# Kernel optimization log

Measured on AMD Instinct MI355X. Metric: run time of the kernel, lower is better.

Reference implementation:

```python
import jax, jax.numpy as jnp
import numpy as np

N, E, D, H = 50000, 800000, 64, 4  # nodes, edges, dim_embedding (=per-head channels), heads
NEG_SLOPE = 0.2
EPS = 1e-16


def _gat(x, src, dst, W, att_src, att_dst, bias, n):
    # x: [N, Din], W: [Din, H*D] -> per-head features [N, H, D]
    xw = (x @ W).reshape(n, H, D)
    a_src = jnp.einsum('nhc,hc->nh', xw, att_src)  # [N, H]
    a_dst = jnp.einsum('nhc,hc->nh', xw, att_dst)
    logits = jax.nn.leaky_relu(a_src[src] + a_dst[dst], NEG_SLOPE)  # [E, H]
    # segment softmax over incoming edges of each destination node
    m = jax.ops.segment_max(logits, dst, num_segments=n)  # [N, H]
    ex = jnp.exp(logits - m[dst])
    s = jax.ops.segment_sum(ex, dst, num_segments=n)
    alpha = ex / (s[dst] + EPS)  # [E, H]
    msg = xw[src] * alpha[..., None]  # [E, H, D]
    out = jax.ops.segment_sum(msg, dst, num_segments=n)  # [N, H, D]
    return out.mean(axis=1) + bias  # concat=False head-mean, [N, D]


def setup_inputs() -> dict:
    key = jax.random.key(0)
    ks = jax.random.split(key, 16)
    sc = 1.0 / np.sqrt(D)
    inp = {
        'x': jax.random.normal(ks[0], (N, D), jnp.float32),
        'edge_index': jax.random.randint(ks[1], (2, E), 0, N, jnp.int64),
    }
    for i, tag in ((2, '1'), (9, '2')):
        inp['W' + tag] = jax.random.normal(ks[i], (D, H * D), jnp.float32) * sc
        inp['att_src' + tag] = jax.random.normal(ks[i + 1], (H, D), jnp.float32) * sc
        inp['att_dst' + tag] = jax.random.normal(ks[i + 2], (H, D), jnp.float32) * sc
        inp['b' + tag] = jnp.zeros((D,), jnp.float32)
        inp['lW' + tag] = jax.random.normal(ks[i + 3], (D, D), jnp.float32) * sc
        inp['lb' + tag] = jnp.zeros((D,), jnp.float32)
    return inp


def reference(x, edge_index, W1, att_src1, att_dst1, b1, lW1, lb1,
              W2, att_src2, att_dst2, b2, lW2, lb2):
    src, dst = edge_index[0], edge_index[1]
    n = x.shape[0]
    h = _gat(x, src, dst, W1, att_src1, att_dst1, b1, n) + (x @ lW1 + lb1)
    h = jax.nn.relu(h)
    out = _gat(h, src, dst, W2, att_src2, att_dst2, b2, n) + (h @ lW2 + lb2)
    return out
```

## Files before the change

kernel.cpp:

```cpp
#include <hip/hip_runtime.h>
#include <math.h>

typedef __attribute__((ext_vector_type(8))) short short8;
typedef __attribute__((ext_vector_type(4))) float f32x4;

#define NBSH 9
#define MAXBIN 128

__device__ inline unsigned fenc(float f){
  unsigned u = __float_as_uint(f);
  return u ^ ((u >> 31) ? 0xFFFFFFFFu : 0x80000000u);
}
__device__ inline float fdec(unsigned k){
  unsigned u = (k & 0x80000000u) ? (k ^ 0x80000000u) : ~k;
  return __uint_as_float(u);
}
__device__ inline unsigned short bf16rne(float f){
  unsigned u = __float_as_uint(f);
  return (unsigned short)((u + 0x7FFFu + ((u >> 16) & 1u)) >> 16);
}

__global__ __launch_bounds__(256) void k_hist(const int* __restrict__ dst, int* __restrict__ deg, int E){
  int e = blockIdx.x*256 + threadIdx.x;
  if (e < E) atomicAdd(&deg[dst[e]], 1);
}

__global__ __launch_bounds__(256) void k_scan(const int* __restrict__ deg, int* __restrict__ offs,
    int* __restrict__ partials, int* __restrict__ flags, int* __restrict__ bincur,
    int nelem, int ndeg){
  __shared__ int sh[256];
  __shared__ int sh2[256];
  int t = threadIdx.x, b = blockIdx.x;
  int i = b*256 + t;
  int v = (i < ndeg) ? deg[i] : 0;
  sh[t] = v; __syncthreads();
  for (int d = 1; d < 256; d <<= 1){
    int add = (t >= d) ? sh[t-d] : 0; __syncthreads();
    sh[t] += add; __syncthreads();
  }
  if (t == 255){
    partials[b] = sh[255];
    __threadfence();
    atomicExch(&flags[b], 1);
  }
  int myp = 0;
  if (t < b){
    while (atomicAdd(&flags[t], 0) == 0){}
    myp = atomicAdd(&partials[t], 0);
  }
  __syncthreads();
  sh2[t] = myp; __syncthreads();
  #pragma unroll
  for (int d = 128; d >= 1; d >>= 1){
    if (t < d) sh2[t] += sh2[t + d];
    __syncthreads();
  }
  int off = sh2[0];
  if (i < nelem){
    int val = off + sh[t] - v;
    offs[i] = val;
    if (i < ndeg && (i & ((1<<NBSH)-1)) == 0) bincur[i >> NBSH] = val;
  }
}

__global__ __launch_bounds__(512) void k_prep(
    const float* __restrict__ W1, const float* __restrict__ as1, const float* __restrict__ ad1,
    const float* __restrict__ b1, const float* __restrict__ lb1, const float* __restrict__ lW1,
    const float* __restrict__ W2, const float* __restrict__ as2, const float* __restrict__ ad2,
    const float* __restrict__ b2, const float* __restrict__ lb2, const float* __restrict__ lW2,
    short* __restrict__ wbigT, short* __restrict__ wattBsw, float* __restrict__ bcomb,
    unsigned* __restrict__ gmax, int4* __restrict__ rec2, int* __restrict__ deg,
    int* __restrict__ flags, int E, int n){
  int L = blockIdx.x;
  const float* W   = L ? W2  : W1;
  const float* asv = L ? as2 : as1;
  const float* adv = L ? ad2 : ad1;
  const float* b   = L ? b2  : b1;
  const float* lb  = L ? lb2 : lb1;
  const float* lW  = L ? lW2 : lW1;
  short* wbT = wbigT  + (size_t)L*64*328;
  short* wsw = wattBsw + L*1024;
  float* bc  = bcomb  + L*64;
  __shared__ float watt[512];
  int t = threadIdx.x;
  { int j = t >> 6, k = t & 63, h = j & 3;
    const float* att = (j < 4) ? asv : adv;
    float s = 0.f;
    for (int c = 0; c < 64; ++c) s += W[k*256 + h*64 + c] * att[h*64 + c];
    watt[j*64 + k] = s; }
  if (t < 8) gmax[t] = 0u;
  if (t < 64) bc[t] = b[t] + lb[t];
  if (L == 0 && t < 16){ int4 z; z.x = 0; z.y = 0; z.z = 0; z.w = 0; rec2[E + t] = z; }
  if (L == 1 && t < 256) flags[t] = 0;
  for (int i = L*512 + t; i < n; i += 1024) deg[i] = 0;
  __syncthreads();
  for (int i = t; i < 1024; i += 512){
    int step = i >> 9, lane = (i >> 3) & 63, j = i & 7;
    int col = lane & 15, q = lane >> 4, k = step*32 + q*8 + j;
    float v = (col < 8) ? watt[col*64 + k] : 0.f;
    wsw[i] = (short)bf16rne(v);
  }
  for (int i = t; i < 64*328; i += 512){
    int c = i / 328, q = i - c*328;
    float val = 0.f;
    if (q < 256){ int hh = q >> 6, cin = q & 63; val = 0.25f * W[cin*256 + hh*64 + c]; }
    else if (q < 320){ int kk = q - 256; val = lW[kk*64 + c]; }
    wbT[i] = (short)bf16rne(val);
  }
}

__global__ __launch_bounds__(256) void k_att(const float* __restrict__ featF,
    const unsigned short* __restrict__ featB, const short* __restrict__ wattBsw,
    float* __restrict__ asrc, float* __restrict__ adst, unsigned short* __restrict__ xbf,
    unsigned* __restrict__ gmax, int n){
  __shared__ unsigned shm[4];
  int t = threadIdx.x;
  if (t < 4) shm[t] = 0u;
  __syncthreads();
  int lane = t & 63, w = t >> 6;
  int nodebase = blockIdx.x*64 + w*16;
  int row16 = lane & 15, q = lane >> 4;
  int rowc = nodebase + row16; if (rowc > n-1) rowc = n-1;
  short8 a0, a1;
  if (featF){
    const float* fp = featF + (size_t)rowc*64;
    float4 c00 = *(const float4*)(fp + q*8);
    float4 c01 = *(const float4*)(fp + q*8 + 4);
    float4 c10 = *(const float4*)(fp + 32 + q*8);
    float4 c11 = *(const float4*)(fp + 32 + q*8 + 4);
    a0[0]=(short)bf16rne(c00.x); a0[1]=(short)bf16rne(c00.y); a0[2]=(short)bf16rne(c00.z); a0[3]=(short)bf16rne(c00.w);
    a0[4]=(short)bf16rne(c01.x); a0[5]=(short)bf16rne(c01.y); a0[6]=(short)bf16rne(c01.z); a0[7]=(short)bf16rne(c01.w);
    a1[0]=(short)bf16rne(c10.x); a1[1]=(short)bf16rne(c10.y); a1[2]=(short)bf16rne(c10.z); a1[3]=(short)bf16rne(c10.w);
    a1[4]=(short)bf16rne(c11.x); a1[5]=(short)bf16rne(c11.y); a1[6]=(short)bf16rne(c11.z); a1[7]=(short)bf16rne(c11.w);
    *(short8*)(xbf + (size_t)rowc*64 + q*8) = a0;
    *(short8*)(xbf + (size_t)rowc*64 + 32 + q*8) = a1;
  } else {
    a0 = *(const short8*)(featB + (size_t)rowc*64 + q*8);
    a1 = *(const short8*)(featB + (size_t)rowc*64 + 32 + q*8);
  }
  short8 b0 = *(const short8*)(wattBsw + lane*8);
  short8 b1 = *(const short8*)(wattBsw + 512 + lane*8);
  f32x4 acc = {0.f,0.f,0.f,0.f};
  acc = __builtin_amdgcn_mfma_f32_16x16x32_bf16(a0, b0, acc, 0, 0, 0);
  acc = __builtin_amdgcn_mfma_f32_16x16x32_bf16(a1, b1, acc, 0, 0, 0);
  int c = lane & 15;
  int rbase = nodebase + q*4;
  if (c < 8){
    float* dstp = (c < 4) ? asrc : adst;
    int hh = c & 3;
    float vmax = -INFINITY;
    #pragma unroll
    for (int r = 0; r < 4; ++r){
      int rr = rbase + r; if (rr > n-1) rr = n-1;
      dstp[(size_t)rr*4 + hh] = acc[r];
      vmax = fmaxf(vmax, acc[r]);
    }
    if (c < 4) atomicMax(&shm[hh], fenc(vmax));
  }
  __syncthreads();
  if (t < 4) atomicMax(gmax + t, shm[t]);
}

__global__ __launch_bounds__(256) void k_scatbin(const int* __restrict__ src, const int* __restrict__ dst,
    const float* __restrict__ asrc, const float* __restrict__ adst,
    int* __restrict__ bincur, const unsigned* __restrict__ gmax,
    int4* __restrict__ rec1, int E){
  __shared__ int hcnt[MAXBIN];
  __shared__ int hbase[MAXBIN];
  int t = threadIdx.x;
  int base = blockIdx.x * 4096 + t;
  if (t < MAXBIN) hcnt[t] = 0;
  __syncthreads();
  int rank[16];
  #pragma unroll
  for (int k = 0; k < 16; ++k){
    int e = base + k*256;
    rank[k] = 0;
    if (e < E){
      int d = dst[e];
      rank[k] = atomicAdd(&hcnt[d >> NBSH], 1);
    }
  }
  __syncthreads();
  if (t < MAXBIN && hcnt[t] > 0) hbase[t] = atomicAdd(&bincur[t], hcnt[t]);
  __syncthreads();
  float gm0 = fdec(gmax[0]), gm1 = fdec(gmax[1]), gm2 = fdec(gmax[2]), gm3 = fdec(gmax[3]);
  #pragma unroll
  for (int k = 0; k < 16; ++k){
    int e = base + k*256;
    if (e < E){
      int d = dst[e], s = src[e];
      float4 as = *(const float4*)(asrc + (size_t)s*4);
      float4 ad = *(const float4*)(adst + (size_t)d*4);
      float g0 = gm0 + ad.x; g0 = fmaxf(g0, 0.2f*g0);
      float g1 = gm1 + ad.y; g1 = fmaxf(g1, 0.2f*g1);
      float g2 = gm2 + ad.z; g2 = fmaxf(g2, 0.2f*g2);
      float g3 = gm3 + ad.w; g3 = fmaxf(g3, 0.2f*g3);
      float l0 = as.x + ad.x; l0 = fmaxf(l0, 0.2f*l0);
      float l1 = as.y + ad.y; l1 = fmaxf(l1, 0.2f*l1);
      float l2 = as.z + ad.z; l2 = fmaxf(l2, 0.2f*l2);
      float l3 = as.w + ad.w; l3 = fmaxf(l3, 0.2f*l3);
      unsigned lo = (unsigned)bf16rne(__expf(l0 - g0)) | ((unsigned)bf16rne(__expf(l1 - g1)) << 16);
      unsigned hi = (unsigned)bf16rne(__expf(l2 - g2)) | ((unsigned)bf16rne(__expf(l3 - g3)) << 16);
      int4 rv; rv.x = (int)lo; rv.y = (int)hi; rv.z = s; rv.w = d;
      rec1[hbase[d >> NBSH] + rank[k]] = rv;
    }
  }
}

__global__ __launch_bounds__(256) void k_place(const int4* __restrict__ rec1,
    const int* __restrict__ offs, int4* __restrict__ rec2, int n){
  __shared__ int cur[1 << NBSH];
  int t = threadIdx.x;
  int nodebase = blockIdx.x << NBSH;
  int nodeend = nodebase + (1 << NBSH); if (nodeend > n) nodeend = n;
  for (int i = t; i < (1 << NBSH); i += 256) cur[i] = 0;
  __syncthreads();
  int winlo = offs[nodebase], winhi = offs[nodeend];
  for (int i = winlo + t; i < winhi; i += 256){
    int4 r = rec1[i];
    int d = r.w;
    int pos = offs[d] + atomicAdd(&cur[d - nodebase], 1);
    rec2[pos] = r;
  }
}

__global__ __launch_bounds__(256) void k_edge2(int4* __restrict__ rec,
    const float* __restrict__ asrc, const float* __restrict__ adst,
    const unsigned* __restrict__ gmax, int E){
  int i = blockIdx.x*256 + threadIdx.x;
  if (i >= E) return;
  int4 r = rec[i];
  int s = r.z, d = r.w;
  float4 as = *(const float4*)(asrc + (size_t)s*4);
  float4 ad = *(const float4*)(adst + (size_t)d*4);
  float g0 = fdec(gmax[0]) + ad.x; g0 = fmaxf(g0, 0.2f*g0);
  float g1 = fdec(gmax[1]) + ad.y; g1 = fmaxf(g1, 0.2f*g1);
  float g2 = fdec(gmax[2]) + ad.z; g2 = fmaxf(g2, 0.2f*g2);
  float g3 = fdec(gmax[3]) + ad.w; g3 = fmaxf(g3, 0.2f*g3);
  float l0 = as.x + ad.x; l0 = fmaxf(l0, 0.2f*l0);
  float l1 = as.y + ad.y; l1 = fmaxf(l1, 0.2f*l1);
  float l2 = as.z + ad.z; l2 = fmaxf(l2, 0.2f*l2);
  float l3 = as.w + ad.w; l3 = fmaxf(l3, 0.2f*l3);
  r.x = (int)((unsigned)bf16rne(__expf(l0 - g0)) | ((unsigned)bf16rne(__expf(l1 - g1)) << 16));
  r.y = (int)((unsigned)bf16rne(__expf(l2 - g2)) | ((unsigned)bf16rne(__expf(l3 - g3)) << 16));
  rec[i] = r;
}

__global__ __launch_bounds__(256) void k_agg(const int4* __restrict__ rec,
    const int* __restrict__ offs, const unsigned short* __restrict__ xbf,
    short* __restrict__ Abf, int n){
  int wid = threadIdx.x >> 6;
  int lane = threadIdx.x & 63;
  int v = blockIdx.x*4 + wid;
  if (v >= n) return;
  int rs = __builtin_amdgcn_readfirstlane(offs[v]);
  int re = __builtin_amdgcn_readfirstlane(offs[v+1]);
  int nrem = re - rs;
  const int4* rp = rec + rs;
  float s0=0.f,s1=0.f,s2=0.f,s3=0.f;
  float a0=0.f,a1=0.f,a2=0.f,a3=0.f;

#define ACC(LO,HI,XU) { \
    float xc = __uint_as_float(((unsigned)(XU)) << 16); \
    float p0 = __uint_as_float((LO) << 16); \
    float p1 = __uint_as_float((LO) & 0xFFFF0000u); \
    float p2 = __uint_as_float((HI) << 16); \
    float p3 = __uint_as_float((HI) & 0xFFFF0000u); \
    s0 += p0; s1 += p1; s2 += p2; s3 += p3; \
    a0 = fmaf(p0, xc, a0); a1 = fmaf(p1, xc, a1); \
    a2 = fmaf(p2, xc, a2); a3 = fmaf(p3, xc, a3); }

  int nch = nrem >> 2;
  if (nch > 0){
    int4 R0[4], R1[4], T[4], U[4];
    unsigned xw0[4], xw1[4];
    #pragma unroll
    for (int j = 0; j < 4; ++j) R0[j] = rp[j];
    #pragma unroll
    for (int j = 0; j < 4; ++j) xw0[j] = xbf[(((size_t)(unsigned)R0[j].z)<<6)+lane];
    #pragma unroll
    for (int j = 0; j < 4; ++j) R1[j] = rp[4+j];
    int c = 0;
    for (; c + 1 < nch; c += 2){
      #pragma unroll
      for (int j = 0; j < 4; ++j) T[j] = rp[((c+2)<<2)+j];
      #pragma unroll
      for (int j = 0; j < 4; ++j) xw1[j] = xbf[(((size_t)(unsigned)R1[j].z)<<6)+lane];
      #pragma unroll
      for (int j = 0; j < 4; ++j) U[j] = rp[((c+3)<<2)+j];
      #pragma unroll
      for (int j = 0; j < 4; ++j) ACC((unsigned)R0[j].x, (unsigned)R0[j].y, xw0[j]);
      #pragma unroll
      for (int j = 0; j < 4; ++j) R0[j] = T[j];
      #pragma unroll
      for (int j = 0; j < 4; ++j) xw0[j] = xbf[(((size_t)(unsigned)R0[j].z)<<6)+lane];
      #pragma unroll
      for (int j = 0; j < 4; ++j) ACC((unsigned)R1[j].x, (unsigned)R1[j].y, xw1[j]);
      #pragma unroll
      for (int j = 0; j < 4; ++j) R1[j] = U[j];
    }
    if (c < nch){
      #pragma unroll
      for (int j = 0; j < 4; ++j) ACC((unsigned)R0[j].x, (unsigned)R0[j].y, xw0[j]);
    }
  }
  for (int i = nch<<2; i < nrem; ++i){
    int4 t = rp[i];
    unsigned xt = xbf[(((size_t)(unsigned)t.z)<<6)+lane];
    ACC((unsigned)t.x, (unsigned)t.y, xt);
  }
#undef ACC
  size_t base = (size_t)v*256 + lane;
  Abf[base +   0] = (short)bf16rne(a0 / (s0 + 1e-16f));
  Abf[base +  64] = (short)bf16rne(a1 / (s1 + 1e-16f));
  Abf[base + 128] = (short)bf16rne(a2 / (s2 + 1e-16f));
  Abf[base + 192] = (short)bf16rne(a3 / (s3 + 1e-16f));
}

__global__ __launch_bounds__(256) void k_out(const short* __restrict__ Abf,
    const unsigned short* __restrict__ xbf, const short* __restrict__ wbigT,
    const float* __restrict__ bcomb, float* __restrict__ outF, unsigned short* __restrict__ outB, int n){
  int lane = threadIdx.x & 63, wid = threadIdx.x >> 6;
  int rowbase = blockIdx.x*64 + wid*16;
  int arow = rowbase + (lane & 15); if (arow > n-1) arow = n-1;
  int ksub = (lane >> 4) * 8;
  const short* ap = Abf + (size_t)arow*256 + ksub;
  const short* xp = (const short*)xbf + (size_t)arow*64 + ksub;
  const short* bp = wbigT + (lane & 15)*328 + ksub;
  f32x4 acc0 = {0.f,0.f,0.f,0.f}, acc1 = acc0, acc2 = acc0, acc3 = acc0;
  #pragma unroll
  for (int k0 = 0; k0 < 320; k0 += 32){
    short8 a  = (k0 < 256) ? *(const short8*)(ap + k0) : *(const short8*)(xp + (k0 - 256));
    short8 b0 = *(const short8*)(bp + k0);
    short8 b1 = *(const short8*)(bp + 16*328 + k0);
    short8 b2 = *(const short8*)(bp + 32*328 + k0);
    short8 b3 = *(const short8*)(bp + 48*328 + k0);
    acc0 = __builtin_amdgcn_mfma_f32_16x16x32_bf16(a, b0, acc0, 0, 0, 0);
    acc1 = __builtin_amdgcn_mfma_f32_16x16x32_bf16(a, b1, acc1, 0, 0, 0);
    acc2 = __builtin_amdgcn_mfma_f32_16x16x32_bf16(a, b2, acc2, 0, 0, 0);
    acc3 = __builtin_amdgcn_mfma_f32_16x16x32_bf16(a, b3, acc3, 0, 0, 0);
  }
  int ccol = lane & 15;
  int crow = rowbase + (lane >> 4)*4;
  float bb0 = bcomb[ 0 + ccol];
  float bb1 = bcomb[16 + ccol];
  float bb2 = bcomb[32 + ccol];
  float bb3 = bcomb[48 + ccol];
  #pragma unroll
  for (int r = 0; r < 4; ++r){
    int rr = crow + r;
    if (rr < n){
      float o0 = acc0[r] + bb0, o1 = acc1[r] + bb1, o2 = acc2[r] + bb2, o3 = acc3[r] + bb3;
      if (outB){
        unsigned short* orow = outB + (size_t)rr*64;
        orow[ 0 + ccol] = bf16rne(fmaxf(o0, 0.f));
        orow[16 + ccol] = bf16rne(fmaxf(o1, 0.f));
        orow[32 + ccol] = bf16rne(fmaxf(o2, 0.f));
        orow[48 + ccol] = bf16rne(fmaxf(o3, 0.f));
      } else {
        float* orow = outF + (size_t)rr*64;
        orow[ 0 + ccol] = o0;
        orow[16 + ccol] = o1;
        orow[32 + ccol] = o2;
        orow[48 + ccol] = o3;
      }
    }
  }
}

extern "C" void kernel_launch(void* const* d_in, const int* in_sizes, int n_in,
                              void* d_out, int out_size, void* d_ws, size_t ws_size,
                              hipStream_t stream){
  const float* x   = (const float*)d_in[0];
  const int*   ei  = (const int*)d_in[1];
  const float* W1  = (const float*)d_in[2];
  const float* as1 = (const float*)d_in[3];
  const float* ad1 = (const float*)d_in[4];
  const float* b1  = (const float*)d_in[5];
  const float* lW1 = (const float*)d_in[6];
  const float* lb1 = (const float*)d_in[7];
  const float* W2  = (const float*)d_in[8];
  const float* as2 = (const float*)d_in[9];
  const float* ad2 = (const float*)d_in[10];
  const float* b2  = (const float*)d_in[11];
  const float* lW2 = (const float*)d_in[12];
  const float* lb2 = (const float*)d_in[13];
  int N = in_sizes[0] / 64;
  int E = in_sizes[1] / 2;
  const int* srce = ei;
  const int* dste = ei + E;

  char* w = (char*)d_ws;
  size_t off = 0;
  auto alloc = [&](size_t bytes)->char*{
    char* p = w + off; off = (off + bytes + 255) & ~(size_t)255; return p;
  };
  int*      offs    = (int*)     alloc((size_t)(N+1)*4);
  int*      deg     = (int*)     alloc((size_t)N*4);
  int*      bincur  = (int*)     alloc(MAXBIN*4);
  int*      partials= (int*)     alloc(256*4);
  int*      flags   = (int*)     alloc(256*4);
  int4*     rec1    = (int4*)    alloc((size_t)E*16);
  int4*     rec2    = (int4*)    alloc((size_t)(E+16)*16);
  short*    wbigT   = (short*)   alloc((size_t)2*64*328*2);
  short*    wattBsw = (short*)   alloc(2*1024*2);
  float*    bcomb   = (float*)   alloc(2*64*4);
  unsigned* gmax    = (unsigned*)alloc(32);
  float*    pasrc   = (float*)   alloc((size_t)N*16);
  float*    padst   = (float*)   alloc((size_t)N*16);
  short*    Abf     = (short*)   alloc((size_t)N*256*2);
  unsigned short* xbf1 = (unsigned short*)alloc((size_t)N*64*2);
  unsigned short* xbf2 = (unsigned short*)alloc((size_t)N*64*2);
  (void)ws_size; (void)n_in; (void)out_size;

  int gE = (E + 255)/256;
  int nelem = N + 1;
  int nb = (nelem + 255)/256;
  int gATT = (N + 63)/64;
  int gOUT = (N + 63)/64;
  int gSB  = (E + 4095)/4096;
  int nbin = (N + (1<<NBSH) - 1) >> NBSH;
  int gAGG = (N + 3)/4;
  float* outp = (float*)d_out;

  k_prep<<<2, 512, 0, stream>>>(W1, as1, ad1, b1, lb1, lW1,
                                W2, as2, ad2, b2, lb2, lW2,
                                wbigT, wattBsw, bcomb, gmax, rec2, deg, flags, E, N);

  k_hist<<<gE, 256, 0, stream>>>(dste, deg, E);
  k_scan<<<nb, 256, 0, stream>>>(deg, offs, partials, flags, bincur, nelem, N);

  k_att <<<gATT, 256, 0, stream>>>(x, nullptr, wattBsw, pasrc, padst, xbf1, gmax, N);
  k_scatbin<<<gSB, 256, 0, stream>>>(srce, dste, pasrc, padst, bincur, gmax, rec1, E);
  k_place<<<nbin, 256, 0, stream>>>(rec1, offs, rec2, N);
  k_agg <<<gAGG, 256, 0, stream>>>(rec2, offs, xbf1, Abf, N);
  k_out <<<gOUT, 256, 0, stream>>>(Abf, xbf1, wbigT, bcomb, nullptr, xbf2, N);

  k_att <<<gATT, 256, 0, stream>>>(nullptr, xbf2, wattBsw + 1024, pasrc, padst, nullptr, gmax + 4, N);
  k_edge2<<<gE, 256, 0, stream>>>(rec2, pasrc, padst, gmax + 4, E);
  k_agg <<<gAGG, 256, 0, stream>>>(rec2, offs, xbf2, Abf, N);
  k_out <<<gOUT, 256, 0, stream>>>(Abf, xbf2, wbigT + 64*328, bcomb + 64, outp, nullptr, N);
}
```

Baseline: 236.4 us.

## Fuse edge aggregation and output MFMA projection into one kernel via LDS tile

```diff
diff --git a/kernel.cpp b/kernel.cpp
--- a/kernel.cpp
+++ b/kernel.cpp
@@ -6,6 +6,7 @@
 
 #define NBSH 9
 #define MAXBIN 128
+#define LROW 264
 
 __device__ inline unsigned fenc(float f){
   unsigned u = __float_as_uint(f);
@@ -247,19 +248,15 @@
   rec[i] = r;
 }
 
-__global__ __launch_bounds__(256) void k_agg(const int4* __restrict__ rec,
+__global__ __launch_bounds__(256) void k_aggout(const int4* __restrict__ rec,
     const int* __restrict__ offs, const unsigned short* __restrict__ xbf,
-    short* __restrict__ Abf, int n){
+    const short* __restrict__ wbigT, const float* __restrict__ bcomb,
+    float* __restrict__ outF, unsigned short* __restrict__ outB, int n){
+  __shared__ __align__(16) short lds[4*16*LROW];
   int wid = threadIdx.x >> 6;
   int lane = threadIdx.x & 63;
-  int v = blockIdx.x*4 + wid;
-  if (v >= n) return;
-  int rs = __builtin_amdgcn_readfirstlane(offs[v]);
-  int re = __builtin_amdgcn_readfirstlane(offs[v+1]);
-  int nrem = re - rs;
-  const int4* rp = rec + rs;
-  float s0=0.f,s1=0.f,s2=0.f,s3=0.f;
-  float a0=0.f,a1=0.f,a2=0.f,a3=0.f;
+  int nodebase = blockIdx.x*64 + wid*16;
+  short* tile = lds + wid*16*LROW;
 
 #define ACC(LO,HI,XU) { \
     float xc = __uint_as_float(((unsigned)(XU)) << 16); \
@@ -271,63 +268,67 @@
     a0 = fmaf(p0, xc, a0); a1 = fmaf(p1, xc, a1); \
     a2 = fmaf(p2, xc, a2); a3 = fmaf(p3, xc, a3); }
 
-  int nch = nrem >> 2;
-  if (nch > 0){
-    int4 R0[4], R1[4], T[4], U[4];
-    unsigned xw0[4], xw1[4];
-    #pragma unroll
-    for (int j = 0; j < 4; ++j) R0[j] = rp[j];
-    #pragma unroll
-    for (int j = 0; j < 4; ++j) xw0[j] = xbf[(((size_t)(unsigned)R0[j].z)<<6)+lane];
-    #pragma unroll
-    for (int j = 0; j < 4; ++j) R1[j] = rp[4+j];
-    int c = 0;
-    for (; c + 1 < nch; c += 2){
+  for (int v16 = 0; v16 < 16; ++v16){
+    int v = nodebase + v16; if (v > n-1) v = n-1;
+    int rs = __builtin_amdgcn_readfirstlane(offs[v]);
+    int re = __builtin_amdgcn_readfirstlane(offs[v+1]);
+    int nrem = re - rs;
+    const int4* rp = rec + rs;
+    float s0=0.f,s1=0.f,s2=0.f,s3=0.f;
+    float a0=0.f,a1=0.f,a2=0.f,a3=0.f;
+    int nch = nrem >> 2;
+    if (nch > 0){
+      int4 R0[4], R1[4], T[4], U[4];
+      unsigned xw0[4], xw1[4];
       #pragma unroll
-      for (int j = 0; j < 4; ++j) T[j] = rp[((c+2)<<2)+j];
-      #pragma unroll
-      for (int j = 0; j < 4; ++j) xw1[j] = xbf[(((size_t)(unsigned)R1[j].z)<<6)+lane];
-      #pragma unroll
-      for (int j = 0; j < 4; ++j) U[j] = rp[((c+3)<<2)+j];
-      #pragma unroll
-      for (int j = 0; j < 4; ++j) ACC((unsigned)R0[j].x, (unsigned)R0[j].y, xw0[j]);
-      #pragma unroll
-      for (int j = 0; j < 4; ++j) R0[j] = T[j];
+      for (int j = 0; j < 4; ++j) R0[j] = rp[j];
       #pragma unroll
       for (int j = 0; j < 4; ++j) xw0[j] = xbf[(((size_t)(unsigned)R0[j].z)<<6)+lane];
       #pragma unroll
-      for (int j = 0; j < 4; ++j) ACC((unsigned)R1[j].x, (unsigned)R1[j].y, xw1[j]);
-      #pragma unroll
-      for (int j = 0; j < 4; ++j) R1[j] = U[j];
-    }
-    if (c < nch){
-      #pragma unroll
-      for (int j = 0; j < 4; ++j) ACC((unsigned)R0[j].x, (unsigned)R0[j].y, xw0[j]);
-    }
-  }
-  for (int i = nch<<2; i < nrem; ++i){
-    int4 t = rp[i];
-    unsigned xt = xbf[(((size_t)(unsigned)t.z)<<6)+lane];
-    ACC((unsigned)t.x, (unsigned)t.y, xt);
+      for (int j = 0; j < 4; ++j) R1[j] = rp[4+j];
+      int c = 0;
+      for (; c + 1 < nch; c += 2){
+        #pragma unroll
+        for (int j = 0; j < 4; ++j) T[j] = rp[((c+2)<<2)+j];
+        #pragma unroll
+        for (int j = 0; j < 4; ++j) xw1[j] = xbf[(((size_t)(unsigned)R1[j].z)<<6)+lane];
+        #pragma unroll
+        for (int j = 0; j < 4; ++j) U[j] = rp[((c+3)<<2)+j];
+        #pragma unroll
+        for (int j = 0; j < 4; ++j) ACC((unsigned)R0[j].x, (unsigned)R0[j].y, xw0[j]);
+        #pragma unroll
+        for (int j = 0; j < 4; ++j) R0[j] = T[j];
+        #pragma unroll
+        for (int j = 0; j < 4; ++j) xw0[j] = xbf[(((size_t)(unsigned)R0[j].z)<<6)+lane];
+        #pragma unroll
+        for (int j = 0; j < 4; ++j) ACC((unsigned)R1[j].x, (unsigned)R1[j].y, xw1[j]);
+        #pragma unroll
+        for (int j = 0; j < 4; ++j) R1[j] = U[j];
+      }
+      if (c < nch){
+        #pragma unroll
+        for (int j = 0; j < 4; ++j) ACC((unsigned)R0[j].x, (unsigned)R0[j].y, xw0[j]);
+      }
+    }
+    for (int i = nch<<2; i < nrem; ++i){
+      int4 t = rp[i];
+      unsigned xt = xbf[(((size_t)(unsigned)t.z)<<6)+lane];
+      ACC((unsigned)t.x, (unsigned)t.y, xt);
+    }
+    short* trow = tile + v16*LROW;
+    trow[lane      ] = (short)bf16rne(a0 / (s0 + 1e-16f));
+    trow[lane +  64] = (short)bf16rne(a1 / (s1 + 1e-16f));
+    trow[lane + 128] = (short)bf16rne(a2 / (s2 + 1e-16f));
+    trow[lane + 192] = (short)bf16rne(a3 / (s3 + 1e-16f));
   }
 #undef ACC
-  size_t base = (size_t)v*256 + lane;
-  Abf[base +   0] = (short)bf16rne(a0 / (s0 + 1e-16f));
-  Abf[base +  64] = (short)bf16rne(a1 / (s1 + 1e-16f));
-  Abf[base + 128] = (short)bf16rne(a2 / (s2 + 1e-16f));
-  Abf[base + 192] = (short)bf16rne(a3 / (s3 + 1e-16f));
-}
-
-__global__ __launch_bounds__(256) void k_out(const short* __restrict__ Abf,
-    const unsigned short* __restrict__ xbf, const short* __restrict__ wbigT,
-    const float* __restrict__ bcomb, float* __restrict__ outF, unsigned short* __restrict__ outB, int n){
-  int lane = threadIdx.x & 63, wid = threadIdx.x >> 6;
-  int rowbase = blockIdx.x*64 + wid*16;
-  int arow = rowbase + (lane & 15); if (arow > n-1) arow = n-1;
-  int ksub = (lane >> 4) * 8;
-  const short* ap = Abf + (size_t)arow*256 + ksub;
+
+  int row16 = lane & 15, q = lane >> 4;
+  int ksub = q*8;
+  int arow = nodebase + row16; if (arow > n-1) arow = n-1;
+  const short* ap = tile + row16*LROW + ksub;
   const short* xp = (const short*)xbf + (size_t)arow*64 + ksub;
-  const short* bp = wbigT + (lane & 15)*328 + ksub;
+  const short* bp = wbigT + row16*328 + ksub;
   f32x4 acc0 = {0.f,0.f,0.f,0.f}, acc1 = acc0, acc2 = acc0, acc3 = acc0;
   #pragma unroll
   for (int k0 = 0; k0 < 320; k0 += 32){
@@ -342,7 +343,7 @@
     acc3 = __builtin_amdgcn_mfma_f32_16x16x32_bf16(a, b3, acc3, 0, 0, 0);
   }
   int ccol = lane & 15;
-  int crow = rowbase + (lane >> 4)*4;
+  int crow = nodebase + q*4;
   float bb0 = bcomb[ 0 + ccol];
   float bb1 = bcomb[16 + ccol];
   float bb2 = bcomb[32 + ccol];
@@ -409,7 +410,6 @@
   unsigned* gmax    = (unsigned*)alloc(32);
   float*    pasrc   = (float*)   alloc((size_t)N*16);
   float*    padst   = (float*)   alloc((size_t)N*16);
-  short*    Abf     = (short*)   alloc((size_t)N*256*2);
   unsigned short* xbf1 = (unsigned short*)alloc((size_t)N*64*2);
   unsigned short* xbf2 = (unsigned short*)alloc((size_t)N*64*2);
   (void)ws_size; (void)n_in; (void)out_size;
@@ -418,10 +418,9 @@
   int nelem = N + 1;
   int nb = (nelem + 255)/256;
   int gATT = (N + 63)/64;
-  int gOUT = (N + 63)/64;
+  int gAO  = (N + 63)/64;
   int gSB  = (E + 4095)/4096;
   int nbin = (N + (1<<NBSH) - 1) >> NBSH;
-  int gAGG = (N + 3)/4;
   float* outp = (float*)d_out;
 
   k_prep<<<2, 512, 0, stream>>>(W1, as1, ad1, b1, lb1, lW1,
@@ -434,11 +433,9 @@
   k_att <<<gATT, 256, 0, stream>>>(x, nullptr, wattBsw, pasrc, padst, xbf1, gmax, N);
   k_scatbin<<<gSB, 256, 0, stream>>>(srce, dste, pasrc, padst, bincur, gmax, rec1, E);
   k_place<<<nbin, 256, 0, stream>>>(rec1, offs, rec2, N);
-  k_agg <<<gAGG, 256, 0, stream>>>(rec2, offs, xbf1, Abf, N);
-  k_out <<<gOUT, 256, 0, stream>>>(Abf, xbf1, wbigT, bcomb, nullptr, xbf2, N);
+  k_aggout<<<gAO, 256, 0, stream>>>(rec2, offs, xbf1, wbigT, bcomb, nullptr, xbf2, N);
 
   k_att <<<gATT, 256, 0, stream>>>(nullptr, xbf2, wattBsw + 1024, pasrc, padst, nullptr, gmax + 4, N);
   k_edge2<<<gE, 256, 0, stream>>>(rec2, pasrc, padst, gmax + 4, E);
-  k_agg <<<gAGG, 256, 0, stream>>>(rec2, offs, xbf2, Abf, N);
-  k_out <<<gOUT, 256, 0, stream>>>(Abf, xbf2, wbigT + 64*328, bcomb + 64, outp, nullptr, N);
-}
+  k_aggout<<<gAO, 256, 0, stream>>>(rec2, offs, xbf2, wbigT + 64*328, bcomb + 64, outp, nullptr, N);
+}
```

Result: slower. 255.0 us (+7.9%).
